# Kernel optimization log

Hardware: AMD Instinct MI355X
Metric: run time of the kernel (lower is better)

Reference implementation:

```python
import jax, jax.numpy as jnp
import numpy as np
from jax import lax

B, H, W = 8, 96, 160
CF = 64        # feature channels (= input_channels//2 = out_channels)
OC = 64        # out channels
K = 3          # kernel
G = 8          # deform (offset) groups
PAD, DIL = 1, 1


def conv3x3(x, w, b):
    y = lax.conv_general_dilated(x, w, (1, 1), ((PAD, PAD), (PAD, PAD)),
                                 dimension_numbers=('NCHW', 'OIHW', 'NCHW'))
    return y + b[None, :, None, None]


def lrelu(x):
    return jnp.where(x >= 0, x, 0.1 * x)


def deform_conv2d(x, offset, mask, w, b):
    # x: (B, Cin, H, W); offset: (B, 2*G*K*K, H, W) in (y, x) per tap; mask: (B, G*K*K, H, W)
    Bq, Cin, Hq, Wq = x.shape
    OCq = w.shape[0]
    off = offset.reshape(Bq, G, K, K, 2, Hq, Wq)
    dy, dx = off[:, :, :, :, 0], off[:, :, :, :, 1]        # (B,G,K,K,H,W)
    ky = jnp.arange(K, dtype=x.dtype).reshape(1, 1, K, 1, 1, 1)
    kx = jnp.arange(K, dtype=x.dtype).reshape(1, 1, 1, K, 1, 1)
    hy = jnp.arange(Hq, dtype=x.dtype).reshape(1, 1, 1, 1, Hq, 1)
    wx = jnp.arange(Wq, dtype=x.dtype).reshape(1, 1, 1, 1, 1, Wq)
    ys = dy + hy - PAD + ky * DIL                          # sampling rows
    xs = dx + wx - PAAD if False else dx + wx - PAD + kx * DIL  # sampling cols
    xg = x.reshape(Bq, G, Cin // G, Hq, Wq)

    def sample(img, ysg, xsg):
        # img: (Cg,H,W); ysg/xsg: (K,K,H,W) -> (Cg,K,K,H,W) bilinear with zero padding
        y0 = jnp.floor(ysg)
        x0 = jnp.floor(xsg)
        wy1 = ysg - y0
        wx1 = xsg - x0
        wy0 = 1.0 - wy1
        wx0 = 1.0 - wx1

        def gather(yi, xi):
            valid = ((yi >= 0) & (yi < Hq) & (xi >= 0) & (xi < Wq)).astype(img.dtype)
            yc = jnp.clip(yi, 0, Hq - 1).astype(jnp.int32)
            xc = jnp.clip(xi, 0, Wq - 1).astype(jnp.int32)
            return img[:, yc, xc] * valid[None]

        return (gather(y0, x0) * (wy0 * wx0)[None]
                + gather(y0, x0 + 1) * (wy0 * wx1)[None]
                + gather(y0 + 1, x0) * (wy1 * wx0)[None]
                + gather(y0 + 1, x0 + 1) * (wy1 * wx1)[None])

    sampled = jax.vmap(jax.vmap(sample))(xg, ys, xs)       # (B,G,Cg,K,K,H,W)
    sampled = sampled * mask.reshape(Bq, G, 1, K, K, Hq, Wq)
    wg = w.reshape(OCq, G, Cin // G, K, K)
    return jnp.einsum('bgcijhw,ogcij->bohw', sampled, wg) + b[None, :, None, None]


def setup_inputs() -> dict:
    key = jax.random.key(0)
    ks = jax.random.split(key, 12)
    cin0 = OC * 3 + 4  # 196

    def u(k, shape, fan_in):
        s = 1.0 / np.sqrt(fan_in)
        return jax.random.uniform(k, shape, jnp.float32, -s, s)

    inp = {
        'current_feature_warped': jax.random.normal(ks[0], (B, CF, H, W), jnp.float32),
        'feat_prop': jax.random.normal(ks[1], (B, CF, H, W), jnp.float32),
        'feat_prev': jax.random.normal(ks[2], (B, CF, H, W), jnp.float32),
        'flow1': jax.random.normal(ks[3], (B, 2, H, W), jnp.float32),
        'flow2': jax.random.normal(ks[4], (B, 2, H, W), jnp.float32),
        'w1': u(ks[5], (OC, cin0, 3, 3), cin0 * 9), 'b1': jnp.zeros((OC,), jnp.float32),
        'w2': u(ks[6], (OC, OC, 3, 3), OC * 9), 'b2': jnp.zeros((OC,), jnp.float32),
        'w3': u(ks[7], (OC, OC, 3, 3), OC * 9), 'b3': jnp.zeros((OC,), jnp.float32),
        'w4': u(ks[8], (K * K * 3 * G, OC, 3, 3), OC * 9), 'b4': jnp.zeros((K * K * 3 * G,), jnp.float32),
        'weight': u(ks[9], (OC, CF, 3, 3), 128 * 9),  # init_weights uses n = input_channels*k*k = 128*9
        'bias': jnp.zeros((OC,), jnp.float32),
    }
    return inp

# remove the accidental typo guard (keeps module exec-clean)
PAAD = PAD


def reference(current_feature_warped, feat_prop, feat_prev, flow1, flow2,
              w1, b1, w2, b2, w3, b3, w4, b4, weight, bias):
    cat = jnp.concatenate([current_feature_warped, feat_prop, feat_prev, flow1, flow2], axis=1)
    o = lrelu(conv3x3(cat, w1, b1))
    o = lrelu(conv3x3(o, w2, b2))
    o = lrelu(conv3x3(o, w3, b3))
    o = conv3x3(o, w4, b4)                                  # (B, 3*G*K*K, H, W)
    offset1, offset2, mask = jnp.split(o, 3, axis=1)        # each (B, G*K*K, H, W)
    rep = offset1.shape[1] // 2                             # G*K*K/2 = 36
    offset1 = offset1 + jnp.tile(flow1[:, ::-1], (1, rep, 1, 1))
    offset2 = offset2 + jnp.tile(flow2[:, ::-1], (1, rep, 1, 1))
    offset = jnp.concatenate([offset1, offset2], axis=1)    # (B, 2*G*K*K, H, W)
    mask = jax.nn.sigmoid(mask)
    return deform_conv2d(current_feature_warped, offset, mask, weight, bias)
```

## Files before the change

### kernel.cpp

```cpp
#include <hip/hip_runtime.h>
#include <hip/hip_bf16.h>
#include <math.h>

typedef __attribute__((ext_vector_type(8))) short short8;
typedef __attribute__((ext_vector_type(4))) float f32x4;

constexpr int B_ = 8, H_ = 96, W_ = 160;
constexpr int HW_ = H_ * W_;
constexpr int NPIX = B_ * HW_;

__device__ __forceinline__ unsigned short f2bf(float f) {
    unsigned int u = __builtin_bit_cast(unsigned int, f);
    u += 0x7FFFu + ((u >> 16) & 1u);
    return (unsigned short)(u >> 16);
}
__device__ __forceinline__ float bf2f(unsigned short s) {
    unsigned int u = ((unsigned int)s) << 16;
    return __builtin_bit_cast(float, u);
}
__device__ __forceinline__ unsigned int cvt_pk_bf16(float lo, float hi) {
    unsigned int r;
    asm volatile("v_cvt_pk_bf16_f32 %0, %1, %2" : "=v"(r) : "v"(lo), "v"(hi));
    return r;
}
__device__ __forceinline__ float f4get(const float4& v, int q) {
    switch (q) { case 0: return v.x; case 1: return v.y;
                 case 2: return v.z; default: return v.w; }
}

__global__ __launch_bounds__(256) void prep_x1(
    const float* __restrict__ cfw, const float* __restrict__ fpro,
    const float* __restrict__ fprv, const float* __restrict__ f1,
    const float* __restrict__ f2, unsigned short* __restrict__ X1)
{
    const int c8 = blockIdx.y;
    const int pix0 = blockIdx.x * 1024 + threadIdx.x * 4;
    unsigned short* dst = X1 + ((size_t)c8 * NPIX + pix0) * 8;

    if (c8 >= 25) {
        uint4 z = {0u, 0u, 0u, 0u};
        #pragma unroll
        for (int q = 0; q < 4; ++q) *(uint4*)(dst + q * 8) = z;
        return;
    }

    const int b  = pix0 / HW_;
    const int hw = pix0 - b * HW_;

    float4 v[8];
    #pragma unroll
    for (int j = 0; j < 8; ++j) {
        int c = c8 * 8 + j;
        const float* src = nullptr; int sc = 0, nc = 0;
        if (c < 64)       { src = cfw;  sc = c;       nc = 64; }
        else if (c < 128) { src = fpro; sc = c - 64;  nc = 64; }
        else if (c < 192) { src = fprv; sc = c - 128; nc = 64; }
        else if (c < 194) { src = f1;   sc = c - 192; nc = 2;  }
        else if (c < 196) { src = f2;   sc = c - 194; nc = 2;  }
        if (src) v[j] = *(const float4*)(src + ((size_t)b * nc + sc) * HW_ + hw);
        else     { v[j].x = v[j].y = v[j].z = v[j].w = 0.f; }
    }
    #pragma unroll
    for (int q = 0; q < 4; ++q) {
        uint4 o;
        o.x = cvt_pk_bf16(f4get(v[0], q), f4get(v[1], q));
        o.y = cvt_pk_bf16(f4get(v[2], q), f4get(v[3], q));
        o.z = cvt_pk_bf16(f4get(v[4], q), f4get(v[5], q));
        o.w = cvt_pk_bf16(f4get(v[6], q), f4get(v[7], q));
        *(uint4*)(dst + q * 8) = o;
    }
}

__device__ __forceinline__ void pack_conv_w(
    const float* __restrict__ w, unsigned short* __restrict__ Bt, int idx,
    int Cin, int KCH, int Nout, int NFTOT)
{
    int lane = idx & 63;
    int r = idx >> 6;
    int nf = r % NFTOT; r /= NFTOT;
    int ck = r % KCH;
    int t  = r / KCH;
    int n  = nf * 16 + (lane & 15);
    int kb = ck * 32 + (lane >> 4) * 8;
    short8 o;
    #pragma unroll
    for (int j = 0; j < 8; ++j) {
        int c = kb + j;
        float v = (c < Cin && n < Nout) ? w[((size_t)n * Cin + c) * 9 + t] : 0.f;
        o[j] = (short)f2bf(v);
    }
    *(short8*)(Bt + (size_t)idx * 8) = o;
}

__global__ __launch_bounds__(256) void prep_wall(
    const float* __restrict__ w1, const float* __restrict__ w2,
    const float* __restrict__ w3, const float* __restrict__ w4,
    const float* __restrict__ wd,
    unsigned short* __restrict__ Bt1, unsigned short* __restrict__ Bt2,
    unsigned short* __restrict__ Bt3, unsigned short* __restrict__ Bt4,
    unsigned short* __restrict__ Btd)
{
    int idx = blockIdx.x * 256 + threadIdx.x;
    if (idx < 16128)      pack_conv_w(w1, Bt1, idx,          196, 7,  64,  4);
    else if (idx < 20736) pack_conv_w(w2, Bt2, idx - 16128,   64, 2,  64,  4);
    else if (idx < 25344) pack_conv_w(w3, Bt3, idx - 20736,   64, 2,  64,  4);
    else if (idx < 41472) pack_conv_w(w4, Bt4, idx - 25344,   64, 2, 216, 14);
    else if (idx < 47616) {
        int id2 = idx - 41472;
        int lane = id2 & 63;
        int r = id2 >> 6;
        int nf = r % 4; r >>= 2;
        int ck = r % 3;
        int g  = r / 3;
        int n  = nf * 16 + (lane & 15);
        int kb = ck * 32 + (lane >> 4) * 8;
        short8 o;
        #pragma unroll
        for (int j = 0; j < 8; ++j) {
            int k = kb + j;
            int t = k >> 3, c = k & 7;
            float v = (t < 9) ? wd[((size_t)n * 64 + g * 8 + c) * 9 + t] : 0.f;
            o[j] = (short)f2bf(v);
        }
        *(short8*)(Btd + (size_t)id2 * 8) = o;
    }
}

template<int KCH, int NFTOT, int NF, bool RELU>
__global__ __launch_bounds__(256) void conv_mfma(
    const unsigned short* __restrict__ X, const unsigned short* __restrict__ Bt,
    const float* __restrict__ bias, unsigned short* __restrict__ Y,
    int CoutTot, int fBase0)
{
    static_assert(NF == 4, "staging assumes 4 KB step chunk");
    __shared__ __align__(16) unsigned short bsh[NF * 512];

    const int tid  = threadIdx.x;
    const int lane = tid & 63;
    const int wv   = tid >> 6;
    const int m0   = blockIdx.x * 128 + wv * 32;
    const int fBase = fBase0 + blockIdx.y * NF;
    const int lm = lane & 15;
    const int l16 = lane >> 4;

    int p[2], hh[2], wp[2];
    #pragma unroll
    for (int mf = 0; mf < 2; ++mf) {
        int pm = m0 + mf * 16 + lm;
        p[mf] = pm;
        hh[mf] = (pm / W_) % H_;
        wp[mf] = pm % W_;
    }

    f32x4 acc[2][NF];
    #pragma unroll
    for (int nf = 0; nf < NF; ++nf) {
        int oc = (fBase + nf) * 16 + lm;
        float bv = (oc < CoutTot) ? bias[oc] : 0.f;
        f32x4 a = {bv, bv, bv, bv};
        acc[0][nf] = a; acc[1][nf] = a;
    }

    const short8 zero = {0,0,0,0,0,0,0,0};
    constexpr int S = KCH * 9;

    uint4 bt = *(const uint4*)(Bt + (size_t)fBase * 512 + tid * 8);

    #pragma unroll
    for (int s = 0; s < S; ++s) {
        const int ck = s / 9, t = s % 9;
        __syncthreads();
        *(uint4*)(bsh + tid * 8) = bt;
        __syncthreads();
        if (s + 1 < S) {
            const int ck2 = (s + 1) / 9, t2 = (s + 1) % 9;
            bt = *(const uint4*)(Bt +
                ((size_t)(t2 * KCH + ck2) * NFTOT + fBase) * 512 + tid * 8);
        }
        const int di = t / 3 - 1, dj = t % 3 - 1;
        const unsigned short* Xp = X + (size_t)(ck * 4 + l16) * NPIX * 8;
        short8 bfr[NF];
        #pragma unroll
        for (int nf = 0; nf < NF; ++nf)
            bfr[nf] = *(const short8*)(bsh + nf * 512 + lane * 8);
        #pragma unroll
        for (int mf = 0; mf < 2; ++mf) {
            bool val = ((unsigned)(hh[mf] + di) < (unsigned)H_) &&
                       ((unsigned)(wp[mf] + dj) < (unsigned)W_);
            const unsigned short* ap = Xp + (size_t)(p[mf] + di * W_ + dj) * 8;
            short8 afr = val ? *(const short8*)ap : zero;
            #pragma unroll
            for (int nf = 0; nf < NF; ++nf)
                acc[mf][nf] = __builtin_amdgcn_mfma_f32_16x16x32_bf16(
                    afr, bfr[nf], acc[mf][nf], 0, 0, 0);
        }
    }

    const int prow = l16 * 4;
    #pragma unroll
    for (int mf = 0; mf < 2; ++mf)
        #pragma unroll
        for (int nf = 0; nf < NF; ++nf) {
            int oc = (fBase + nf) * 16 + lm;
            if (oc < CoutTot) {
                #pragma unroll
                for (int r = 0; r < 4; ++r) {
                    int pix = m0 + mf * 16 + prow + r;
                    float v = acc[mf][nf][r];
                    if (RELU) v = (v >= 0.f) ? v : 0.1f * v;
                    Y[((size_t)(oc >> 3) * NPIX + pix) * 8 + (oc & 7)] = f2bf(v);
                }
            }
        }
}

template<int HALF>
__global__ __launch_bounds__(256, 4) void conv4_mfma(
    const unsigned short* __restrict__ X, const unsigned short* __restrict__ Bt,
    const float* __restrict__ bias,
    unsigned short* __restrict__ oY, unsigned short* __restrict__ oX,
    unsigned short* __restrict__ oM)
{
    __shared__ __align__(16) unsigned short bsh[7 * 512];

    const int tid  = threadIdx.x;
    const int lane = tid & 63;
    const int wv   = tid >> 6;
    const int pix0 = blockIdx.x * 128;
    const int m0   = pix0 + wv * 32;
    const int lm = lane & 15;
    const int l16 = lane >> 4;
    constexpr int FB = HALF * 7;

    int p[2], hh[2], wp[2];
    #pragma unroll
    for (int mf = 0; mf < 2; ++mf) {
        int pm = m0 + mf * 16 + lm;
        p[mf] = pm;
        hh[mf] = (pm / W_) % H_;
        wp[mf] = pm % W_;
    }

    f32x4 acc[2][7];
    #pragma unroll
    for (int nf = 0; nf < 7; ++nf) {
        int oc = (FB + nf) * 16 + lm;
        float bv = (oc < 216) ? bias[oc] : 0.f;
        f32x4 a = {bv, bv, bv, bv};
        acc[0][nf] = a; acc[1][nf] = a;
    }

    const short8 zero = {0,0,0,0,0,0,0,0};
    const bool two = (tid < 192);

    uint4 bt0 = *(const uint4*)(Bt + (size_t)FB * 512 + tid * 8);
    uint4 bt1 = {0u, 0u, 0u, 0u};
    if (two) bt1 = *(const uint4*)(Bt + (size_t)FB * 512 + (256 + tid) * 8);

    #pragma unroll
    for (int s = 0; s < 18; ++s) {
        const int ck = s / 9, t = s % 9;
        __syncthreads();
        *(uint4*)(bsh + tid * 8) = bt0;
        if (two) *(uint4*)(bsh + (256 + tid) * 8) = bt1;
        __syncthreads();
        if (s + 1 < 18) {
            const int ck2 = (s + 1) / 9, t2 = (s + 1) % 9;
            const unsigned short* nb =
                Bt + ((size_t)((t2 * 2 + ck2) * 14 + FB)) * 512;
            bt0 = *(const uint4*)(nb + tid * 8);
            if (two) bt1 = *(const uint4*)(nb + (256 + tid) * 8);
        }
        const int di = t / 3 - 1, dj = t % 3 - 1;
        const unsigned short* Xp = X + (size_t)(ck * 4 + l16) * NPIX * 8;
        short8 afr[2];
        #pragma unroll
        for (int mf = 0; mf < 2; ++mf) {
            bool val = ((unsigned)(hh[mf] + di) < (unsigned)H_) &&
                       ((unsigned)(wp[mf] + dj) < (unsigned)W_);
            const unsigned short* ap = Xp + (size_t)(p[mf] + di * W_ + dj) * 8;
            afr[mf] = val ? *(const short8*)ap : zero;
        }
        #pragma unroll
        for (int nf = 0; nf < 7; ++nf) {
            short8 bfr = *(const short8*)(bsh + nf * 512 + lane * 8);
            acc[0][nf] = __builtin_amdgcn_mfma_f32_16x16x32_bf16(
                afr[0], bfr, acc[0][nf], 0, 0, 0);
            acc[1][nf] = __builtin_amdgcn_mfma_f32_16x16x32_bf16(
                afr[1], bfr, acc[1][nf], 0, 0, 0);
        }
    }

    const int prow = l16 * 4;
    #pragma unroll
    for (int mf = 0; mf < 2; ++mf) {
        const int pixb = m0 + mf * 16 + prow;
        #pragma unroll
        for (int nf = 0; nf < 7; ++nf) {
            const int nfg = FB + nf;
            const int oc = nfg * 16 + lm;
            if (nfg < 9) {
                const int pr = nfg * 8 + (lm >> 1);
                unsigned short* plane = ((lm & 1) ? oX : oY) + (size_t)pr * NPIX;
                uint2 sv;
                sv.x = cvt_pk_bf16(acc[mf][nf][0], acc[mf][nf][1]);
                sv.y = cvt_pk_bf16(acc[mf][nf][2], acc[mf][nf][3]);
                *(uint2*)(plane + pixb) = sv;
            } else if (oc < 216) {
                const int mi = (nfg - 9) * 16 + lm;
                float v0 = 1.f / (1.f + expf(-acc[mf][nf][0]));
                float v1 = 1.f / (1.f + expf(-acc[mf][nf][1]));
                float v2 = 1.f / (1.f + expf(-acc[mf][nf][2]));
                float v3 = 1.f / (1.f + expf(-acc[mf][nf][3]));
                uint2 sv;
                sv.x = cvt_pk_bf16(v0, v1);
                sv.y = cvt_pk_bf16(v2, v3);
                *(uint2*)(oM + (size_t)mi * NPIX + pixb) = sv;
            }
        }
    }
}

__global__ __launch_bounds__(256) void deform_mfma(
    const unsigned short* __restrict__ Xg,
    const unsigned short* __restrict__ oY,
    const unsigned short* __restrict__ oX,
    const unsigned short* __restrict__ oM,
    const float* __restrict__ f1, const float* __restrict__ f2,
    const unsigned short* __restrict__ Btd,
    const float* __restrict__ bia,
    float* __restrict__ out)
{
    __shared__ __align__(16) char lds[64 * 256];

    const int tid  = threadIdx.x;
    const int lane = tid & 63;
    const int wv   = tid >> 6;
    const int lm   = lane & 15;
    const int l16  = lane >> 4;
    const int pix0 = blockIdx.x * 64;
    const int b    = pix0 / HW_;
    const int hw0  = pix0 % HW_;

    const int pix = tid & 63;
    const int hw  = hw0 + pix;
    const int h   = hw / W_;
    const int w   = hw - h * W_;
    const size_t gp = (size_t)(pix0 + pix);
    const size_t bF = (size_t)b * 2 * HW_;

    {
        uint4 z = {0u, 0u, 0u, 0u};
        #pragma unroll
        for (int i = 0; i < 4; ++i)
            ((uint4*)lds)[i * 256 + tid] = z;
    }

    f32x4 acc[4];
    {
        float bv = bia[wv * 16 + lm];
        f32x4 a = {bv, bv, bv, bv};
        #pragma unroll
        for (int mf = 0; mf < 4; ++mf) acc[mf] = a;
    }

    for (int g = 0; g < 8; ++g) {
        const unsigned short* Xp = Xg + (size_t)g * NPIX * 8;
        __syncthreads();

        const float* fl = (g < 4) ? f1 : f2;
        const float fy = fl[bF + (size_t)HW_ + hw];
        const float fx = fl[bF + hw];
        unsigned short uy[3], ux[3], um[3];
        #pragma unroll
        for (int it = 0; it < 3; ++it) {
            int t = wv + 4 * it;
            bool act = (it < 2) || (wv == 0);
            if (act) {
                size_t po = (size_t)(g * 9 + t) * NPIX + gp;
                uy[it] = oY[po]; ux[it] = oX[po]; um[it] = oM[po];
            }
        }
        #pragma unroll
        for (int it = 0; it < 3; ++it) {
            int t = wv + 4 * it;
            bool act = (it < 2) || (wv == 0);
            if (act) {
                float dy = bf2f(uy[it]) + fy;
                float dx = bf2f(ux[it]) + fx;
                float m  = bf2f(um[it]);

                float ys = dy + (float)(h - 1 + t / 3);
                float xs = dx + (float)(w - 1 + t % 3);
                float y0f = floorf(ys), x0f = floorf(xs);
                float wy1 = ys - y0f, wx1 = xs - x0f;
                float wy0 = 1.f - wy1, wx0 = 1.f - wx1;
                int iy0 = (int)y0f, ix0 = (int)x0f;
                int iy1 = iy0 + 1,  ix1 = ix0 + 1;
                bool vy0 = (unsigned)iy0 < (unsigned)H_;
                bool vy1 = (unsigned)iy1 < (unsigned)H_;
                bool vx0 = (unsigned)ix0 < (unsigned)W_;
                bool vx1 = (unsigned)ix1 < (unsigned)W_;
                int cy0 = min(max(iy0, 0), H_ - 1), cy1 = min(max(iy1, 0), H_ - 1);
                int cx0 = min(max(ix0, 0), W_ - 1), cx1 = min(max(ix1, 0), W_ - 1);
                float w00 = (vy0 && vx0) ? wy0 * wx0 * m : 0.f;
                float w01 = (vy0 && vx1) ? wy0 * wx1 * m : 0.f;
                float w10 = (vy1 && vx0) ? wy1 * wx0 * m : 0.f;
                float w11 = (vy1 && vx1) ? wy1 * wx1 * m : 0.f;

                size_t r0 = (size_t)b * HW_ + (size_t)cy0 * W_;
                size_t r1 = (size_t)b * HW_ + (size_t)cy1 * W_;
                uint4 c00 = *(const uint4*)(Xp + (r0 + cx0) * 8);
                uint4 c01 = *(const uint4*)(Xp + (r0 + cx1) * 8);
                uint4 c10 = *(const uint4*)(Xp + (r1 + cx0) * 8);
                uint4 c11 = *(const uint4*)(Xp + (r1 + cx1) * 8);

                float a8[8];
                #pragma unroll
                for (int i = 0; i < 8; ++i) a8[i] = 0.f;
                const unsigned int u00[4] = {c00.x, c00.y, c00.z, c00.w};
                const unsigned int u01[4] = {c01.x, c01.y, c01.z, c01.w};
                const unsigned int u10[4] = {c10.x, c10.y, c10.z, c10.w};
                const unsigned int u11[4] = {c11.x, c11.y, c11.z, c11.w};
                #pragma unroll
                for (int i = 0; i < 4; ++i) {
                    a8[2*i]   += w00 * __builtin_bit_cast(float, u00[i] << 16);
                    a8[2*i+1] += w00 * __builtin_bit_cast(float, u00[i] & 0xFFFF0000u);
                    a8[2*i]   += w01 * __builtin_bit_cast(float, u01[i] << 16);
                    a8[2*i+1] += w01 * __builtin_bit_cast(float, u01[i] & 0xFFFF0000u);
                    a8[2*i]   += w10 * __builtin_bit_cast(float, u10[i] << 16);
                    a8[2*i+1] += w10 * __builtin_bit_cast(float, u10[i] & 0xFFFF0000u);
                    a8[2*i]   += w11 * __builtin_bit_cast(float, u11[i] << 16);
                    a8[2*i+1] += w11 * __builtin_bit_cast(float, u11[i] & 0xFFFF0000u);
                }
                uint4 ov;
                ov.x = cvt_pk_bf16(a8[0], a8[1]);
                ov.y = cvt_pk_bf16(a8[2], a8[3]);
                ov.z = cvt_pk_bf16(a8[4], a8[5]);
                ov.w = cvt_pk_bf16(a8[6], a8[7]);
                int slot = t ^ (pix & 7);
                *(uint4*)(lds + pix * 256 + slot * 16) = ov;
            }
        }
        __syncthreads();
        #pragma unroll
        for (int ck = 0; ck < 3; ++ck) {
            short8 bfr = ((const short8*)Btd)[((size_t)(g * 3 + ck) * 4 + wv) * 64 + lane];
            const int slotbase = ck * 4 + l16;
            #pragma unroll
            for (int mf = 0; mf < 4; ++mf) {
                int row = mf * 16 + lm;
                int slot = slotbase ^ (lm & 7);
                short8 afr = *(const short8*)(lds + row * 256 + slot * 16);
                acc[mf] = __builtin_amdgcn_mfma_f32_16x16x32_bf16(
                    afr, bfr, acc[mf], 0, 0, 0);
            }
        }
    }

    const int oc = wv * 16 + lm;
    #pragma unroll
    for (int mf = 0; mf < 4; ++mf) {
        int px = hw0 + mf * 16 + l16 * 4;
        *(f32x4*)(out + (size_t)(b * 64 + oc) * HW_ + px) = acc[mf];
    }
}

extern "C" void kernel_launch(void* const* d_in, const int* in_sizes, int n_in,
                              void* d_out, int out_size, void* d_ws, size_t ws_size,
                              hipStream_t stream)
{
    const float* cfw  = (const float*)d_in[0];
    const float* fpro = (const float*)d_in[1];
    const float* fprv = (const float*)d_in[2];
    const float* fl1  = (const float*)d_in[3];
    const float* fl2  = (const float*)d_in[4];
    const float* w1   = (const float*)d_in[5];
    const float* b1   = (const float*)d_in[6];
    const float* w2   = (const float*)d_in[7];
    const float* b2   = (const float*)d_in[8];
    const float* w3   = (const float*)d_in[9];
    const float* b3   = (const float*)d_in[10];
    const float* w4   = (const float*)d_in[11];
    const float* b4   = (const float*)d_in[12];
    const float* wdef = (const float*)d_in[13];
    const float* bdef = (const float*)d_in[14];
    float* out = (float*)d_out;

    char* ws = (char*)d_ws;
    unsigned short* X1  = (unsigned short*)(ws);
    unsigned short* buf1= (unsigned short*)(ws + 55050240);
    unsigned short* o2  = (unsigned short*)(ws + 70778880);
    unsigned short* oY  = (unsigned short*)(ws + 70778880);
    unsigned short* oX  = oY + (size_t)72 * NPIX;
    unsigned short* oM  = oX + (size_t)72 * NPIX;
    unsigned short* Bt1 = (unsigned short*)(ws + 125829120);
    unsigned short* Bt2 = (unsigned short*)(ws + 125829120 + 258048);
    unsigned short* Bt3 = (unsigned short*)(ws + 125829120 + 258048 + 73728);
    unsigned short* Bt4 = (unsigned short*)(ws + 125829120 + 258048 + 2*73728);
    unsigned short* Btd = (unsigned short*)(ws + 125829120 + 2*258048 + 2*73728);

    prep_x1<<<dim3(NPIX / 1024, 28), dim3(256), 0, stream>>>(
        cfw, fpro, fprv, fl1, fl2, X1);
    prep_wall<<<dim3((47616 + 255) / 256), dim3(256), 0, stream>>>(
        w1, w2, w3, w4, wdef, Bt1, Bt2, Bt3, Bt4, Btd);

    dim3 blk(256);
    dim3 gridM(NPIX / 128, 1);
    conv_mfma<7, 4, 4, true><<<gridM, blk, 0, stream>>>(X1, Bt1, b1, buf1, 64, 0);
    conv_mfma<2, 4, 4, true><<<gridM, blk, 0, stream>>>(buf1, Bt2, b2, o2, 64, 0);
    conv_mfma<2, 4, 4, true><<<gridM, blk, 0, stream>>>(o2, Bt3, b3, buf1, 64, 0);
    conv4_mfma<0><<<gridM, blk, 0, stream>>>(buf1, Bt4, b4, oY, oX, oM);
    conv4_mfma<1><<<gridM, blk, 0, stream>>>(buf1, Bt4, b4, oY, oX, oM);
    deform_mfma<<<dim3(NPIX / 64), blk, 0, stream>>>(
        X1, oY, oX, oM, fl1, fl2, Btd, bdef, out);
}
```

Before: 252.3 us.

## Stage all nine tap weight chunks per channel block to cut barriers

```diff
diff --git a/kernel.cpp b/kernel.cpp
--- a/kernel.cpp
+++ b/kernel.cpp
@@ -127,13 +127,13 @@
 }
 
 template<int KCH, int NFTOT, int NF, bool RELU>
-__global__ __launch_bounds__(256) void conv_mfma(
+__global__ __launch_bounds__(256, 4) void conv_mfma(
     const unsigned short* __restrict__ X, const unsigned short* __restrict__ Bt,
     const float* __restrict__ bias, unsigned short* __restrict__ Y,
     int CoutTot, int fBase0)
 {
-    static_assert(NF == 4, "staging assumes 4 KB step chunk");
-    __shared__ __align__(16) unsigned short bsh[NF * 512];
+    static_assert(NF == 4, "staging assumes 4 KB per tap chunk");
+    __shared__ __align__(16) unsigned short bsh[9 * 2048];
 
     const int tid  = threadIdx.x;
     const int lane = tid & 63;
@@ -162,37 +162,44 @@
     }
 
     const short8 zero = {0,0,0,0,0,0,0,0};
-    constexpr int S = KCH * 9;
-
-    uint4 bt = *(const uint4*)(Bt + (size_t)fBase * 512 + tid * 8);
-
-    #pragma unroll
-    for (int s = 0; s < S; ++s) {
-        const int ck = s / 9, t = s % 9;
+
+    uint4 breg[9];
+    #pragma unroll
+    for (int j = 0; j < 9; ++j)
+        breg[j] = *(const uint4*)(Bt +
+            ((size_t)(j * KCH) * NFTOT + fBase) * 512 + tid * 8);
+
+    for (int ck = 0; ck < KCH; ++ck) {
         __syncthreads();
-        *(uint4*)(bsh + tid * 8) = bt;
+        #pragma unroll
+        for (int j = 0; j < 9; ++j)
+            *(uint4*)(bsh + j * 2048 + tid * 8) = breg[j];
         __syncthreads();
-        if (s + 1 < S) {
-            const int ck2 = (s + 1) / 9, t2 = (s + 1) % 9;
-            bt = *(const uint4*)(Bt +
-                ((size_t)(t2 * KCH + ck2) * NFTOT + fBase) * 512 + tid * 8);
-        }
-        const int di = t / 3 - 1, dj = t % 3 - 1;
+        if (ck + 1 < KCH) {
+            #pragma unroll
+            for (int j = 0; j < 9; ++j)
+                breg[j] = *(const uint4*)(Bt +
+                    ((size_t)(j * KCH + ck + 1) * NFTOT + fBase) * 512 + tid * 8);
+        }
         const unsigned short* Xp = X + (size_t)(ck * 4 + l16) * NPIX * 8;
-        short8 bfr[NF];
-        #pragma unroll
-        for (int nf = 0; nf < NF; ++nf)
-            bfr[nf] = *(const short8*)(bsh + nf * 512 + lane * 8);
-        #pragma unroll
-        for (int mf = 0; mf < 2; ++mf) {
-            bool val = ((unsigned)(hh[mf] + di) < (unsigned)H_) &&
-                       ((unsigned)(wp[mf] + dj) < (unsigned)W_);
-            const unsigned short* ap = Xp + (size_t)(p[mf] + di * W_ + dj) * 8;
-            short8 afr = val ? *(const short8*)ap : zero;
+        #pragma unroll
+        for (int t = 0; t < 9; ++t) {
+            const int di = t / 3 - 1, dj = t % 3 - 1;
+            short8 bfr[NF];
             #pragma unroll
             for (int nf = 0; nf < NF; ++nf)
-                acc[mf][nf] = __builtin_amdgcn_mfma_f32_16x16x32_bf16(
-                    afr, bfr[nf], acc[mf][nf], 0, 0, 0);
+                bfr[nf] = *(const short8*)(bsh + t * 2048 + nf * 512 + lane * 8);
+            #pragma unroll
+            for (int mf = 0; mf < 2; ++mf) {
+                bool val = ((unsigned)(hh[mf] + di) < (unsigned)H_) &&
+                           ((unsigned)(wp[mf] + dj) < (unsigned)W_);
+                const unsigned short* ap = Xp + (size_t)(p[mf] + di * W_ + dj) * 8;
+                short8 afr = val ? *(const short8*)ap : zero;
+                #pragma unroll
+                for (int nf = 0; nf < NF; ++nf)
+                    acc[mf][nf] = __builtin_amdgcn_mfma_f32_16x16x32_bf16(
+                        afr, bfr[nf], acc[mf][nf], 0, 0, 0);
+            }
         }
     }
 
```

Result: slower. 362.6 us (+43.8%).
